# Optimization experiments

Hardware: AMD Instinct MI355X
Metric: run time of the kernel (lower is better)

The kernel has to match this reference:

```python
import jax, jax.numpy as jnp
import numpy as np

D_MODEL = 1024
NUM_HEADS = 16
HEAD_DIM = D_MODEL // NUM_HEADS
NEG_INF = -1e9


def setup_inputs() -> dict:
    key = jax.random.key(0)
    ks = jax.random.split(key, 9)
    B, S, SI = 4, 1024, 512
    scale = 1.0 / np.sqrt(D_MODEL)
    return {
        "hidden_states": jax.random.normal(ks[0], (B, S, D_MODEL), jnp.float32),
        "image_hidden_states": jax.random.normal(ks[1], (B, SI, D_MODEL), jnp.float32),
        "attention_mask": jax.random.randint(ks[2], (B, 1, S, S + SI), 0, 2, jnp.int32),
        "w_q": jax.random.normal(ks[3], (D_MODEL, D_MODEL), jnp.float32) * scale,
        "w_k": jax.random.normal(ks[4], (D_MODEL, D_MODEL), jnp.float32) * scale,
        "w_v": jax.random.normal(ks[5], (D_MODEL, D_MODEL), jnp.float32) * scale,
        "u_k": jax.random.normal(ks[6], (D_MODEL, D_MODEL), jnp.float32) * scale,
        "u_v": jax.random.normal(ks[7], (D_MODEL, D_MODEL), jnp.float32) * scale,
        "w_o": jax.random.normal(ks[8], (D_MODEL, D_MODEL), jnp.float32) * scale,
    }


def _split_heads(x):
    # [B, S, D] -> [B, H, S, Dh]
    B, S, _ = x.shape
    return x.reshape(B, S, NUM_HEADS, HEAD_DIM).transpose(0, 2, 1, 3)


def reference(hidden_states, image_hidden_states, attention_mask,
              w_q, w_k, w_v, u_k, u_v, w_o):
    # nn.Linear(bias=False): y = x @ W.T
    q = _split_heads(hidden_states @ w_q.T)          # [B,H,S,Dh]
    k = _split_heads(hidden_states @ w_k.T)          # [B,H,S,Dh]
    v = _split_heads(hidden_states @ w_v.T)
    k_img = _split_heads(image_hidden_states @ u_k.T)  # [B,H,SI,Dh]
    v_img = _split_heads(image_hidden_states @ u_v.T)
    k = jnp.concatenate([k, k_img], axis=2)          # [B,H,S+SI,Dh]
    v = jnp.concatenate([v, v_img], axis=2)

    scores = jnp.einsum('bhqd,bhkd->bhqk', q, k) / np.sqrt(HEAD_DIM)
    scores = jnp.where(attention_mask == 0, NEG_INF, scores)
    p_attn = jax.nn.softmax(scores, axis=-1)         # dropout p=0.0 (eval)
    x = jnp.einsum('bhqk,bhkd->bhqd', p_attn, v)     # [B,H,S,Dh]
    B, H, S, Dh = x.shape
    x = x.transpose(0, 2, 1, 3).reshape(B, S, D_MODEL)
    return x @ w_o.T
```

## Files before the change

### kernel.cpp

```cpp
#include <hip/hip_runtime.h>
#include <stdint.h>


typedef unsigned short u16;
typedef short bf16x8v __attribute__((ext_vector_type(8)));
typedef float f32x4 __attribute__((ext_vector_type(4)));

__device__ __forceinline__ u16 f2bf(float f) {
  union { float f; uint32_t u; } x; x.f = f;
  uint32_t r = x.u + 0x7FFFu + ((x.u >> 16) & 1u);
  return (u16)(r >> 16);
}

__device__ __forceinline__ uint32_t cvtpk(float a, float b) {
  uint32_t r;
  asm("v_cvt_pk_bf16_f32 %0, %1, %2" : "=v"(r) : "v"(a), "v"(b));
  return r;
}

__device__ __forceinline__ float maskand(float e, uint32_t msrc, int off) {
  uint32_t mm = (uint32_t)((int32_t)(msrc << (31 - off)) >> 31);
  union { float f; uint32_t u; } x; x.f = e; x.u &= mm; return x.f;
}

__device__ __forceinline__ void gl_lds16(const u16* g, u16* l) {
  __builtin_amdgcn_global_load_lds((const __attribute__((address_space(1))) unsigned int*)g,
                                   (__attribute__((address_space(3))) unsigned int*)l,
                                   16, 0, 0);
}

__global__ __launch_bounds__(512, 2) void gemm_qkv(
    const float* __restrict__ Hs, const float* __restrict__ Im,
    const float* __restrict__ Wq, const float* __restrict__ Wk, const float* __restrict__ Wv,
    const float* __restrict__ Uk, const float* __restrict__ Uv,
    const int* __restrict__ Mk,
    u16* __restrict__ Qd, u16* __restrict__ Kd, u16* __restrict__ Vd,
    uint32_t* __restrict__ Mw)
{
  __shared__ __align__(16) u16 As[2 * 16384];
  __shared__ __align__(16) u16 Bs[2 * 16384];
  const int hb = blockIdx.x;
  const int xcd = hb & 7, slot = hb >> 3;
  int bid = (slot < 24) ? xcd * 24 + slot : 192 + xcd * 8 + (slot - 24);
  const float *Ap, *Bp;
  int bm, bn, mode;
  if (bid < 192) { mode = 4; bm = (bid / 12) * 256; bn = (bid % 12) * 256;
                   Ap = Hs + (size_t)bm * 1024;
                   Bp = ((bn < 1024) ? Wq : (bn < 2048) ? Wk : Wv) + (size_t)(bn & 1023) * 1024; }
  else           { mode = 5; int r = bid - 192; bm = (r >> 3) * 256; bn = (r & 7) * 256;
                   Ap = Im + (size_t)bm * 1024;
                   Bp = ((bn < 1024) ? Uk : Uv) + (size_t)(bn & 1023) * 1024; }
  const int tid = threadIdx.x, lane = tid & 63, wave = tid >> 6;
  const int wr = wave >> 2, wc = wave & 3;
  const int g = lane >> 4, c = lane & 15, cs = c & 7;
  const int srow = tid >> 3;
  const int pch  = tid & 7;
  const int gsw  = (pch ^ (srow & 7)) * 8;

  f32x4 zf = {0.f, 0.f, 0.f, 0.f};
  f32x4 acc[8][4];
  #pragma unroll
  for (int f = 0; f < 8; ++f)
    #pragma unroll
    for (int nf = 0; nf < 4; ++nf) acc[f][nf] = zf;

  float4 sa[4][2], sb[4][2];

  #define LOAD_A(kt)                                                               \
    _Pragma("unroll")                                                              \
    for (int j_ = 0; j_ < 4; ++j_) {                                               \
      const float* p_ = Ap + (size_t)(j_ * 64 + srow) * 1024 + (kt) * 64 + gsw;    \
      sa[j_][0] = *(const float4*)p_;                                              \
      sa[j_][1] = *(const float4*)(p_ + 4);                                        \
    }
  #define LOAD_B(kt)                                                               \
    _Pragma("unroll")                                                              \
    for (int j_ = 0; j_ < 4; ++j_) {                                               \
      const float* p_ = Bp + (size_t)(j_ * 64 + srow) * 1024 + (kt) * 64 + gsw;    \
      sb[j_][0] = *(const float4*)p_;                                              \
      sb[j_][1] = *(const float4*)(p_ + 4);                                        \
    }
  #define CVT_A(buf)                                                               \
    _Pragma("unroll")                                                              \
    for (int j_ = 0; j_ < 4; ++j_) {                                               \
      uint4 w_;                                                                    \
      w_.x = cvtpk(sa[j_][0].x, sa[j_][0].y);                                      \
      w_.y = cvtpk(sa[j_][0].z, sa[j_][0].w);                                      \
      w_.z = cvtpk(sa[j_][1].x, sa[j_][1].y);                                      \
      w_.w = cvtpk(sa[j_][1].z, sa[j_][1].w);                                      \
      *(uint4*)&As[(buf) + (j_ * 64 + srow) * 64 + pch * 8] = w_;                  \
    }
  #define CVT_B(buf)                                                               \
    _Pragma("unroll")                                                              \
    for (int j_ = 0; j_ < 4; ++j_) {                                               \
      uint4 w_;                                                                    \
      w_.x = cvtpk(sb[j_][0].x, sb[j_][0].y);                                      \
      w_.y = cvtpk(sb[j_][0].z, sb[j_][0].w);                                      \
      w_.z = cvtpk(sb[j_][1].x, sb[j_][1].y);                                      \
      w_.w = cvtpk(sb[j_][1].z, sb[j_][1].w);                                      \
      *(uint4*)&Bs[(buf) + (j_ * 64 + srow) * 64 + pch * 8] = w_;                  \
    }

  LOAD_A(0); LOAD_B(0);
  {
    const int fid = hb * 512 + tid;
    #pragma unroll 1
    for (int w = fid; w < 196608; w += 131072) {
      const int4* p = (const int4*)(Mk + (size_t)w * 32);
      uint32_t bits = 0;
      #pragma unroll 1
      for (int h_ = 0; h_ < 2; ++h_) {
        int4 v0 = p[h_ * 4 + 0], v1 = p[h_ * 4 + 1];
        int4 v2 = p[h_ * 4 + 2], v3 = p[h_ * 4 + 3];
        int bo = h_ * 16;
        bits |= (uint32_t)(v0.x != 0) << (bo + 0);
        bits |= (uint32_t)(v0.y != 0) << (bo + 1);
        bits |= (uint32_t)(v0.z != 0) << (bo + 2);
        bits |= (uint32_t)(v0.w != 0) << (bo + 3);
        bits |= (uint32_t)(v1.x != 0) << (bo + 4);
        bits |= (uint32_t)(v1.y != 0) << (bo + 5);
        bits |= (uint32_t)(v1.z != 0) << (bo + 6);
        bits |= (uint32_t)(v1.w != 0) << (bo + 7);
        bits |= (uint32_t)(v2.x != 0) << (bo + 8);
        bits |= (uint32_t)(v2.y != 0) << (bo + 9);
        bits |= (uint32_t)(v2.z != 0) << (bo + 10);
        bits |= (uint32_t)(v2.w != 0) << (bo + 11);
        bits |= (uint32_t)(v3.x != 0) << (bo + 12);
        bits |= (uint32_t)(v3.y != 0) << (bo + 13);
        bits |= (uint32_t)(v3.z != 0) << (bo + 14);
        bits |= (uint32_t)(v3.w != 0) << (bo + 15);
      }
      Mw[w] = bits;
    }
  }
  CVT_A(0);  CVT_B(0);
  __syncthreads();

  for (int kt = 0; kt < 16; ++kt) {
    const int bc = (kt & 1) * 16384;
    const int bx = bc ^ 16384;
    if (kt < 15) LOAD_A(kt + 1);

    bf16x8v Bf[4][2];
    #pragma unroll
    for (int nf = 0; nf < 4; ++nf)
      #pragma unroll
      for (int ks = 0; ks < 2; ++ks)
        Bf[nf][ks] = *(const bf16x8v*)&Bs[bc + (wc * 64 + nf * 16 + c) * 64 + ((ks * 4 + g) ^ cs) * 8];

    #pragma unroll
    for (int p = 0; p < 4; ++p) {
      bf16x8v Af[2][2];
      #pragma unroll
      for (int i = 0; i < 2; ++i)
        #pragma unroll
        for (int ks = 0; ks < 2; ++ks)
          Af[i][ks] = *(const bf16x8v*)&As[bc + (wr * 128 + (p * 2 + i) * 16 + c) * 64 + ((ks * 4 + g) ^ cs) * 8];
      __builtin_amdgcn_s_setprio(1);
      #pragma unroll
      for (int i = 0; i < 2; ++i)
        #pragma unroll
        for (int nf = 0; nf < 4; ++nf)
          #pragma unroll
          for (int ks = 0; ks < 2; ++ks)
            acc[p * 2 + i][nf] =
              __builtin_amdgcn_mfma_f32_16x16x32_bf16(Af[i][ks], Bf[nf][ks], acc[p * 2 + i][nf], 0, 0, 0);
      __builtin_amdgcn_s_setprio(0);
      if (p == 1 && kt < 15) {
        __builtin_amdgcn_sched_barrier(0);
        CVT_A(bx);
        LOAD_B(kt + 1);
        __builtin_amdgcn_sched_barrier(0);
      }
    }
    if (kt < 15) {
      __builtin_amdgcn_sched_barrier(0);
      CVT_B(bx);
    }
    __syncthreads();
  }
  #undef LOAD_A
  #undef LOAD_B
  #undef CVT_A
  #undef CVT_B

  const int gn0 = bn + wc * 64;
  if (mode == 4) {
    if (bn < 1024) {
      #pragma unroll
      for (int f = 0; f < 8; ++f)
        #pragma unroll
        for (int nf = 0; nf < 4; ++nf) {
          int gm = bm + wr * 128 + f * 16 + 4 * g;
          int gn = gn0 + nf * 16 + c;
          #pragma unroll
          for (int j = 0; j < 4; ++j)
            Qd[(size_t)(gm + j) * 1024 + gn] = f2bf(acc[f][nf][j] * 0.18033688011112042f);
        }
    } else if (bn < 2048) {
      #pragma unroll
      for (int f = 0; f < 8; ++f)
        #pragma unroll
        for (int nf = 0; nf < 4; ++nf) {
          int gm = bm + wr * 128 + f * 16 + 4 * g;
          int b_ = gm >> 10, s_ = gm & 1023;
          int gn = gn0 - 1024 + nf * 16 + c;
          #pragma unroll
          for (int j = 0; j < 4; ++j)
            Kd[(size_t)(b_ * 1536 + s_ + j) * 1024 + gn] = f2bf(acc[f][nf][j]);
        }
    } else {
      #pragma unroll
      for (int f = 0; f < 8; ++f)
        #pragma unroll
        for (int nf = 0; nf < 4; ++nf) {
          int gm = bm + wr * 128 + f * 16 + 4 * g;
          int b_ = gm >> 10, s_ = gm & 1023;
          int d_ = gn0 - 2048 + nf * 16 + c;
          uint2 st;
          st.x = cvtpk(acc[f][nf][0], acc[f][nf][1]);
          st.y = cvtpk(acc[f][nf][2], acc[f][nf][3]);
          *(uint2*)&Vd[(size_t)(b_ * 1024 + d_) * 1536 + s_] = st;
        }
    }
  } else {
    if (bn < 1024) {
      #pragma unroll
      for (int f = 0; f < 8; ++f)
        #pragma unroll
        for (int nf = 0; nf < 4; ++nf) {
          int gm = bm + wr * 128 + f * 16 + 4 * g;
          int b_ = gm >> 9, s_ = gm & 511;
          int gn = gn0 + nf * 16 + c;
          #pragma unroll
          for (int j = 0; j < 4; ++j)
            Kd[(size_t)(b_ * 1536 + 1024 + s_ + j) * 1024 + gn] = f2bf(acc[f][nf][j]);
        }
    } else {
      #pragma unroll
      for (int f = 0; f < 8; ++f)
        #pragma unroll
        for (int nf = 0; nf < 4; ++nf) {
          int gm = bm + wr * 128 + f * 16 + 4 * g;
          int b_ = gm >> 9, s_ = gm & 511;
          int d_ = gn0 - 1024 + nf * 16 + c;
          uint2 st;
          st.x = cvtpk(acc[f][nf][0], acc[f][nf][1]);
          st.y = cvtpk(acc[f][nf][2], acc[f][nf][3]);
          *(uint2*)&Vd[(size_t)(b_ * 1024 + d_) * 1536 + 1024 + s_] = st;
        }
    }
  }
}

__global__ __launch_bounds__(256) void gemm_out(const u16* __restrict__ A, const float* __restrict__ Bw,
                                                float* __restrict__ Cout)
{
  __shared__ __align__(16) u16 As2[2 * 8192];
  __shared__ __align__(16) u16 Bs2[2 * 8192];
  const int hb = blockIdx.x;
  const int xcd = hb & 7, slot = hb >> 3;
  const int rg = xcd * 4 + (slot >> 3);
  const int cg = slot & 7;
  const int bm = rg * 128, bn = cg * 128;
  const int tid  = threadIdx.x;
  const int lane = tid & 63, wave = tid >> 6;
  const int wr = wave >> 1, wc = wave & 1;
  const int g = lane >> 4, c = lane & 15, cs = c & 7;
  const int sr  = tid >> 3;
  const int pch = tid & 7;
  const int gsw = (pch ^ (sr & 7)) * 8;

  f32x4 zf = {0.f, 0.f, 0.f, 0.f};
  f32x4 acc[4][4];
  #pragma unroll
  for (int mi = 0; mi < 4; ++mi)
    #pragma unroll
    for (int ni = 0; ni < 4; ++ni) acc[mi][ni] = zf;

  float4 sb[4][2];

  #define STG_A(buf, kt)                                                           \
    _Pragma("unroll")                                                              \
    for (int q_ = 0; q_ < 4; ++q_) {                                               \
      int row_ = q_ * 32 + sr;                                                     \
      gl_lds16(A + (size_t)(bm + row_) * 1024 + (kt) * 64 + gsw,                   \
               &As2[(buf) + row_ * 64 + pch * 8]);                                 \
    }
  #define LOAD_B(kt)                                                               \
    _Pragma("unroll")                                                              \
    for (int q_ = 0; q_ < 4; ++q_) {                                               \
      const float* p_ = Bw + (size_t)(bn + q_ * 32 + sr) * 1024 + (kt) * 64 + gsw; \
      sb[q_][0] = *(const float4*)p_;                                              \
      sb[q_][1] = *(const float4*)(p_ + 4);                                        \
    }
  #define CVT_B(buf)                                                               \
    _Pragma("unroll")                                                              \
    for (int q_ = 0; q_ < 4; ++q_) {                                               \
      uint4 w_;                                                                    \
      w_.x = cvtpk(sb[q_][0].x, sb[q_][0].y);                                      \
      w_.y = cvtpk(sb[q_][0].z, sb[q_][0].w);                                      \
      w_.z = cvtpk(sb[q_][1].x, sb[q_][1].y);                                      \
      w_.w = cvtpk(sb[q_][1].z, sb[q_][1].w);                                      \
      *(uint4*)&Bs2[(buf) + (q_ * 32 + sr) * 64 + pch * 8] = w_;                   \
    }

  STG_A(0, 0);
  LOAD_B(0);
  CVT_B(0);
  __syncthreads();

  for (int kt = 0; kt < 16; ++kt) {
    const int bc = (kt & 1) * 8192;
    const int bx = bc ^ 8192;
    if (kt < 15) { STG_A(bx, kt + 1); LOAD_B(kt + 1); }

    #pragma unroll
    for (int ks = 0; ks < 2; ++ks) {
      bf16x8v af[4], bfr[4];
      #pragma unroll
      for (int mi = 0; mi < 4; ++mi)
        af[mi] = *(const bf16x8v*)&As2[bc + (wr * 64 + mi * 16 + c) * 64 + ((ks * 4 + g) ^ cs) * 8];
      #pragma unroll
      for (int ni = 0; ni < 4; ++ni)
        bfr[ni] = *(const bf16x8v*)&Bs2[bc + (wc * 64 + ni * 16 + c) * 64 + ((ks * 4 + g) ^ cs) * 8];
      __builtin_amdgcn_s_setprio(1);
      #pragma unroll
      for (int mi = 0; mi < 4; ++mi)
        #pragma unroll
        for (int ni = 0; ni < 4; ++ni)
          acc[mi][ni] = __builtin_amdgcn_mfma_f32_16x16x32_bf16(af[mi], bfr[ni], acc[mi][ni], 0, 0, 0);
      __builtin_amdgcn_s_setprio(0);
    }
    if (kt < 15) {
      __builtin_amdgcn_sched_barrier(0);
      CVT_B(bx);
    }
    __syncthreads();
  }
  #undef STG_A
  #undef LOAD_B
  #undef CVT_B

  #pragma unroll
  for (int mi = 0; mi < 4; ++mi)
    #pragma unroll
    for (int ni = 0; ni < 4; ++ni)
      #pragma unroll
      for (int j = 0; j < 4; ++j) {
        int gm = bm + wr * 64 + mi * 16 + 4 * g + j;
        int gn = bn + wc * 64 + ni * 16 + c;
        Cout[(size_t)gm * 1024 + gn] = acc[mi][ni][j];
      }
}

__global__ __launch_bounds__(256) void attn_kernel(const u16* __restrict__ Q, const u16* __restrict__ Kc,
                                                   const u16* __restrict__ Vt,
                                                   const uint32_t* __restrict__ Mw,
                                                   u16* __restrict__ AO)
{
  const int bid = blockIdx.x;
  const int grp = bid & 63;
  const int qt  = bid >> 6;
  const int h = grp & 15, b = grp >> 4;
  const int q0 = qt * 64;
  const int tid = threadIdx.x, lane = tid & 63, wave = tid >> 6;
  const int g = lane >> 4, c = lane & 15;
  const int qw = q0 + wave * 16;

  __shared__ __align__(16) u16 Ks[64 * 64];
  __shared__ __align__(16) u16 Vs[64 * 64];
  __shared__ __align__(16) u16 Ps[4][16 * 72];

  bf16x8v qf0, qf1;
  {
    const u16* qp = Q + (size_t)(b * 1024 + qw + c) * 1024 + h * 64 + g * 8;
    qf0 = *(const bf16x8v*)qp;
    qf1 = *(const bf16x8v*)(qp + 32);
  }
  f32x4 zf = {0.f, 0.f, 0.f, 0.f};
  f32x4 O[4];
  float l = 0.f;
  #pragma unroll
  for (int dt = 0; dt < 4; ++dt) O[dt] = zf;

  const int sr  = tid >> 3;
  const int pch = tid & 7;
  const int swz = (pch ^ (sr & 7)) * 8;
  const int cs  = c & 7;
  const u16* Kbase = Kc + (size_t)(b * 1536) * 1024 + h * 64;
  const u16* Vbase = Vt + (size_t)(b * 1024 + h * 64) * 1536;
  const uint32_t* mrow = Mw + (size_t)(b * 1024 + qw + c) * 48;

  bf16x8v kr0, kr1, vr0, vr1;
  kr0 = *(const bf16x8v*)(Kbase + (size_t)sr * 1024 + pch * 8);
  kr1 = *(const bf16x8v*)(Kbase + (size_t)(32 + sr) * 1024 + pch * 8);
  vr0 = *(const bf16x8v*)(Vbase + (size_t)sr * 1536 + pch * 8);
  vr1 = *(const bf16x8v*)(Vbase + (size_t)(32 + sr) * 1536 + pch * 8);
  *(bf16x8v*)&Ks[sr * 64 + swz]        = kr0;
  *(bf16x8v*)&Ks[(32 + sr) * 64 + swz] = kr1;
  *(bf16x8v*)&Vs[sr * 64 + swz]        = vr0;
  *(bf16x8v*)&Vs[(32 + sr) * 64 + swz] = vr1;
  __syncthreads();

  for (int kt = 0; kt < 24; ++kt) {
    if (kt < 23) {
      const int ln = (kt + 1) * 64;
      kr0 = *(const bf16x8v*)(Kbase + (size_t)(ln + sr) * 1024 + pch * 8);
      kr1 = *(const bf16x8v*)(Kbase + (size_t)(ln + 32 + sr) * 1024 + pch * 8);
      vr0 = *(const bf16x8v*)(Vbase + (size_t)sr * 1536 + ln + pch * 8);
      vr1 = *(const bf16x8v*)(Vbase + (size_t)(32 + sr) * 1536 + ln + pch * 8);
    }
    uint2 mwv = *(const uint2*)(mrow + kt * 2);

    f32x4 s[4];
    __builtin_amdgcn_s_setprio(1);
    #pragma unroll
    for (int nt = 0; nt < 4; ++nt) {
      const u16* kr = &Ks[(nt * 16 + c) * 64];
      bf16x8v k0 = *(const bf16x8v*)&kr[(g ^ cs) * 8];
      bf16x8v k1 = *(const bf16x8v*)&kr[((4 + g) ^ cs) * 8];
      f32x4 z = zf;
      z = __builtin_amdgcn_mfma_f32_16x16x32_bf16(k0, qf0, z, 0, 0, 0);
      z = __builtin_amdgcn_mfma_f32_16x16x32_bf16(k1, qf1, z, 0, 0, 0);
      s[nt] = z;
    }
    __builtin_amdgcn_s_setprio(0);

    uint64_t mq = (((uint64_t)mwv.y << 32) | (uint64_t)mwv.x) >> (4 * g);
    uint32_t mlo = (uint32_t)mq, mhi = (uint32_t)(mq >> 32);
    #pragma unroll
    for (int nt = 0; nt < 4; ++nt) {
      uint32_t msrc = (nt < 2) ? mlo : mhi;
      #pragma unroll
      for (int j = 0; j < 4; ++j) {
        float e = exp2f(s[nt][j]);
        float p = maskand(e, msrc, 16 * (nt & 1) + j);
        s[nt][j] = p;
        l += p;
      }
    }

    u16* pw = &Ps[wave][0];
    #pragma unroll
    for (int nt = 0; nt < 4; ++nt) {
      uint2 pk2;
      pk2.x = cvtpk(s[nt][0], s[nt][1]);
      pk2.y = cvtpk(s[nt][2], s[nt][3]);
      *(uint2*)&pw[c * 72 + nt * 16 + g * 4] = pk2;
    }
    bf16x8v pb0 = *(const bf16x8v*)&pw[c * 72 + g * 8];
    bf16x8v pb1 = *(const bf16x8v*)&pw[c * 72 + 32 + g * 8];
    __builtin_amdgcn_s_setprio(1);
    #pragma unroll
    for (int dt = 0; dt < 4; ++dt) {
      const u16* vr = &Vs[(dt * 16 + c) * 64];
      bf16x8v v0 = *(const bf16x8v*)&vr[(g ^ cs) * 8];
      bf16x8v v1 = *(const bf16x8v*)&vr[((4 + g) ^ cs) * 8];
      O[dt] = __builtin_amdgcn_mfma_f32_16x16x32_bf16(v0, pb0, O[dt], 0, 0, 0);
      O[dt] = __builtin_amdgcn_mfma_f32_16x16x32_bf16(v1, pb1, O[dt], 0, 0, 0);
    }
    __builtin_amdgcn_s_setprio(0);

    __syncthreads();
    if (kt < 23) {
      *(bf16x8v*)&Ks[sr * 64 + swz]        = kr0;
      *(bf16x8v*)&Ks[(32 + sr) * 64 + swz] = kr1;
      *(bf16x8v*)&Vs[sr * 64 + swz]        = vr0;
      *(bf16x8v*)&Vs[(32 + sr) * 64 + swz] = vr1;
      __syncthreads();
    }
  }

  float r = l;
  r += __shfl_xor(r, 16);
  r += __shfl_xor(r, 32);
  float inv = 1.f / r;
  size_t ro = (size_t)(b * 1024 + qw + c) * 1024 + h * 64;
  #pragma unroll
  for (int dt = 0; dt < 4; ++dt) {
    uint2 st;
    st.x = cvtpk(O[dt][0] * inv, O[dt][1] * inv);
    st.y = cvtpk(O[dt][2] * inv, O[dt][3] * inv);
    *(uint2*)&AO[ro + dt * 16 + 4 * g] = st;
  }
}

extern "C" void kernel_launch(void* const* d_in, const int* in_sizes, int n_in,
                              void* d_out, int out_size, void* d_ws, size_t ws_size,
                              hipStream_t stream) {
  (void)in_sizes; (void)n_in; (void)out_size; (void)ws_size;
  const float* hs = (const float*)d_in[0];
  const float* im = (const float*)d_in[1];
  const int*   mk = (const int*)d_in[2];
  const float* wq = (const float*)d_in[3];
  const float* wk = (const float*)d_in[4];
  const float* wv = (const float*)d_in[5];
  const float* uk = (const float*)d_in[6];
  const float* uv = (const float*)d_in[7];
  const float* wo = (const float*)d_in[8];

  char* ws = (char*)d_ws;
  u16* Qb  = (u16*)(ws + 0);
  u16* Kb  = (u16*)(ws + 8388608);
  u16* Vtb = (u16*)(ws + 20971520);
  u16* AO  = (u16*)(ws + 33554432);
  uint32_t* Mw = (uint32_t*)(ws + 41943040);

  gemm_qkv<<<256, 512, 0, stream>>>(hs, im, wq, wk, wv, uk, uv, mk, Qb, Kb, Vtb, Mw);
  attn_kernel<<<1024, 256, 0, stream>>>(Qb, Kb, Vtb, Mw, AO);
  gemm_out<<<256, 256, 0, stream>>>(AO, wo, (float*)d_out);
}
```

Baseline: 133.7 us.

## Double-buffer attention K/V tiles via direct global-to-LDS loads; hoist GEMM B prefetch

The attention kernel now keeps two LDS buffers for K and V and fills the next tile with direct global-to-LDS loads (gl_lds16) while computing on the current one. This drops the register staging and one of the two barriers per iteration, and the swizzle moves from the LDS address to the global source address. The GEMM kernel also issues the B-tile prefetch at the top of the iteration next to the A prefetch, instead of midway through. The cost is twice the K/V LDS footprint, which may lower occupancy. The change also relies on a gl_lds16 helper that must already be defined in the hidden part of the file.

```diff
diff --git a/kernel.cpp b/kernel.cpp
--- a/kernel.cpp
+++ b/kernel.cpp
@@ -139,7 +139,7 @@
   for (int kt = 0; kt < 16; ++kt) {
     const int bc = (kt & 1) * 16384;
     const int bx = bc ^ 16384;
-    if (kt < 15) LOAD_A(kt + 1);
+    if (kt < 15) { LOAD_A(kt + 1); LOAD_B(kt + 1); }
 
     bf16x8v Bf[4][2];
     #pragma unroll
@@ -169,7 +169,6 @@
       if (p == 1 && kt < 15) {
         __builtin_amdgcn_sched_barrier(0);
         CVT_A(bx);
-        LOAD_B(kt + 1);
         __builtin_amdgcn_sched_barrier(0);
       }
     }
@@ -368,8 +367,8 @@
   const int g = lane >> 4, c = lane & 15;
   const int qw = q0 + wave * 16;
 
-  __shared__ __align__(16) u16 Ks[64 * 64];
-  __shared__ __align__(16) u16 Vs[64 * 64];
+  __shared__ __align__(16) u16 Ks[2][64 * 64];
+  __shared__ __align__(16) u16 Vs[2][64 * 64];
   __shared__ __align__(16) u16 Ps[4][16 * 72];
 
   bf16x8v qf0, qf1;
@@ -392,32 +391,27 @@
   const u16* Vbase = Vt + (size_t)(b * 1024 + h * 64) * 1536;
   const uint32_t* mrow = Mw + (size_t)(b * 1024 + qw + c) * 48;
 
-  bf16x8v kr0, kr1, vr0, vr1;
-  kr0 = *(const bf16x8v*)(Kbase + (size_t)sr * 1024 + pch * 8);
-  kr1 = *(const bf16x8v*)(Kbase + (size_t)(32 + sr) * 1024 + pch * 8);
-  vr0 = *(const bf16x8v*)(Vbase + (size_t)sr * 1536 + pch * 8);
-  vr1 = *(const bf16x8v*)(Vbase + (size_t)(32 + sr) * 1536 + pch * 8);
-  *(bf16x8v*)&Ks[sr * 64 + swz]        = kr0;
-  *(bf16x8v*)&Ks[(32 + sr) * 64 + swz] = kr1;
-  *(bf16x8v*)&Vs[sr * 64 + swz]        = vr0;
-  *(bf16x8v*)&Vs[(32 + sr) * 64 + swz] = vr1;
+  #define ATTN_STAGE(bf, l0)                                                      \
+    do {                                                                          \
+      gl_lds16(Kbase + (size_t)((l0) + sr) * 1024 + swz,      &Ks[bf][sr * 64 + pch * 8]);        \
+      gl_lds16(Kbase + (size_t)((l0) + 32 + sr) * 1024 + swz, &Ks[bf][(32 + sr) * 64 + pch * 8]); \
+      gl_lds16(Vbase + (size_t)sr * 1536 + (l0) + swz,        &Vs[bf][sr * 64 + pch * 8]);        \
+      gl_lds16(Vbase + (size_t)(32 + sr) * 1536 + (l0) + swz, &Vs[bf][(32 + sr) * 64 + pch * 8]); \
+    } while (0)
+
+  ATTN_STAGE(0, 0);
   __syncthreads();
 
   for (int kt = 0; kt < 24; ++kt) {
-    if (kt < 23) {
-      const int ln = (kt + 1) * 64;
-      kr0 = *(const bf16x8v*)(Kbase + (size_t)(ln + sr) * 1024 + pch * 8);
-      kr1 = *(const bf16x8v*)(Kbase + (size_t)(ln + 32 + sr) * 1024 + pch * 8);
-      vr0 = *(const bf16x8v*)(Vbase + (size_t)sr * 1536 + ln + pch * 8);
-      vr1 = *(const bf16x8v*)(Vbase + (size_t)(32 + sr) * 1536 + ln + pch * 8);
-    }
+    const int bc = kt & 1, bx = bc ^ 1;
+    if (kt < 23) ATTN_STAGE(bx, (kt + 1) * 64);
     uint2 mwv = *(const uint2*)(mrow + kt * 2);
 
     f32x4 s[4];
     __builtin_amdgcn_s_setprio(1);
     #pragma unroll
     for (int nt = 0; nt < 4; ++nt) {
-      const u16* kr = &Ks[(nt * 16 + c) * 64];
+      const u16* kr = &Ks[bc][(nt * 16 + c) * 64];
       bf16x8v k0 = *(const bf16x8v*)&kr[(g ^ cs) * 8];
       bf16x8v k1 = *(const bf16x8v*)&kr[((4 + g) ^ cs) * 8];
       f32x4 z = zf;
@@ -454,7 +448,7 @@
     __builtin_amdgcn_s_setprio(1);
     #pragma unroll
     for (int dt = 0; dt < 4; ++dt) {
-      const u16* vr = &Vs[(dt * 16 + c) * 64];
+      const u16* vr = &Vs[bc][(dt * 16 + c) * 64];
       bf16x8v v0 = *(const bf16x8v*)&vr[(g ^ cs) * 8];
       bf16x8v v1 = *(const bf16x8v*)&vr[((4 + g) ^ cs) * 8];
       O[dt] = __builtin_amdgcn_mfma_f32_16x16x32_bf16(v0, pb0, O[dt], 0, 0, 0);
@@ -462,15 +456,9 @@
     }
     __builtin_amdgcn_s_setprio(0);
 
-    __syncthreads();
-    if (kt < 23) {
-      *(bf16x8v*)&Ks[sr * 64 + swz]        = kr0;
-      *(bf16x8v*)&Ks[(32 + sr) * 64 + swz] = kr1;
-      *(bf16x8v*)&Vs[sr * 64 + swz]        = vr0;
-      *(bf16x8v*)&Vs[(32 + sr) * 64 + swz] = vr1;
-      __syncthreads();
-    }
-  }
+    if (kt < 23) __syncthreads();
+  }
+  #undef ATTN_STAGE
 
   float r = l;
   r += __shfl_xor(r, 16);
```

Result: slower. 151.4 us (+13.2%).

## Split attention over two key halves and merge the partial results

Applied to the files above, without the earlier changes.

The attention kernel now splits the 24 key tiles into two halves, launching twice as many blocks. Each block writes an unnormalized bf16 partial output and a per-row partial sum. A new merge kernel adds the two partials, divides by the combined sum, and writes the result into the reused Q buffer that the output GEMM then reads. The aim is more parallelism and shorter per-block serial loops, at the cost of an extra launch, roughly 16MB of extra partial traffic, and bf16 rounding of the unnormalized partials.

```diff
diff --git a/kernel.cpp b/kernel.cpp
--- a/kernel.cpp
+++ b/kernel.cpp
@@ -357,16 +357,21 @@
 __global__ __launch_bounds__(256) void attn_kernel(const u16* __restrict__ Q, const u16* __restrict__ Kc,
                                                    const u16* __restrict__ Vt,
                                                    const uint32_t* __restrict__ Mw,
-                                                   u16* __restrict__ AO)
+                                                   u16* __restrict__ Op0, u16* __restrict__ Op1,
+                                                   float* __restrict__ Lp0, float* __restrict__ Lp1)
 {
   const int bid = blockIdx.x;
   const int grp = bid & 63;
-  const int qt  = bid >> 6;
+  const int qt  = (bid >> 6) & 15;
+  const int half = bid >> 10;
   const int h = grp & 15, b = grp >> 4;
   const int q0 = qt * 64;
   const int tid = threadIdx.x, lane = tid & 63, wave = tid >> 6;
   const int g = lane >> 4, c = lane & 15;
   const int qw = q0 + wave * 16;
+  u16*  Op = half ? Op1 : Op0;
+  float* Lp = half ? Lp1 : Lp0;
+  const int kt0 = half * 12;
 
   __shared__ __align__(16) u16 Ks[64 * 64];
   __shared__ __align__(16) u16 Vs[64 * 64];
@@ -393,18 +398,21 @@
   const uint32_t* mrow = Mw + (size_t)(b * 1024 + qw + c) * 48;
 
   bf16x8v kr0, kr1, vr0, vr1;
-  kr0 = *(const bf16x8v*)(Kbase + (size_t)sr * 1024 + pch * 8);
-  kr1 = *(const bf16x8v*)(Kbase + (size_t)(32 + sr) * 1024 + pch * 8);
-  vr0 = *(const bf16x8v*)(Vbase + (size_t)sr * 1536 + pch * 8);
-  vr1 = *(const bf16x8v*)(Vbase + (size_t)(32 + sr) * 1536 + pch * 8);
+  {
+    const int l0 = kt0 * 64;
+    kr0 = *(const bf16x8v*)(Kbase + (size_t)(l0 + sr) * 1024 + pch * 8);
+    kr1 = *(const bf16x8v*)(Kbase + (size_t)(l0 + 32 + sr) * 1024 + pch * 8);
+    vr0 = *(const bf16x8v*)(Vbase + (size_t)sr * 1536 + l0 + pch * 8);
+    vr1 = *(const bf16x8v*)(Vbase + (size_t)(32 + sr) * 1536 + l0 + pch * 8);
+  }
   *(bf16x8v*)&Ks[sr * 64 + swz]        = kr0;
   *(bf16x8v*)&Ks[(32 + sr) * 64 + swz] = kr1;
   *(bf16x8v*)&Vs[sr * 64 + swz]        = vr0;
   *(bf16x8v*)&Vs[(32 + sr) * 64 + swz] = vr1;
   __syncthreads();
 
-  for (int kt = 0; kt < 24; ++kt) {
-    if (kt < 23) {
+  for (int kt = kt0; kt < kt0 + 12; ++kt) {
+    if (kt < kt0 + 11) {
       const int ln = (kt + 1) * 64;
       kr0 = *(const bf16x8v*)(Kbase + (size_t)(ln + sr) * 1024 + pch * 8);
       kr1 = *(const bf16x8v*)(Kbase + (size_t)(ln + 32 + sr) * 1024 + pch * 8);
@@ -463,7 +471,7 @@
     __builtin_amdgcn_s_setprio(0);
 
     __syncthreads();
-    if (kt < 23) {
+    if (kt < kt0 + 11) {
       *(bf16x8v*)&Ks[sr * 64 + swz]        = kr0;
       *(bf16x8v*)&Ks[(32 + sr) * 64 + swz] = kr1;
       *(bf16x8v*)&Vs[sr * 64 + swz]        = vr0;
@@ -475,15 +483,39 @@
   float r = l;
   r += __shfl_xor(r, 16);
   r += __shfl_xor(r, 32);
-  float inv = 1.f / r;
-  size_t ro = (size_t)(b * 1024 + qw + c) * 1024 + h * 64;
+  const int row = b * 1024 + qw + c;
+  if (lane < 16) Lp[(size_t)row * 16 + h] = r;
+  size_t ro = (size_t)row * 1024 + h * 64;
   #pragma unroll
   for (int dt = 0; dt < 4; ++dt) {
     uint2 st;
-    st.x = cvtpk(O[dt][0] * inv, O[dt][1] * inv);
-    st.y = cvtpk(O[dt][2] * inv, O[dt][3] * inv);
-    *(uint2*)&AO[ro + dt * 16 + 4 * g] = st;
-  }
+    st.x = cvtpk(O[dt][0], O[dt][1]);
+    st.y = cvtpk(O[dt][2], O[dt][3]);
+    *(uint2*)&Op[ro + dt * 16 + 4 * g] = st;
+  }
+}
+
+__global__ __launch_bounds__(256) void attn_merge(const u16* __restrict__ Op0, const u16* __restrict__ Op1,
+                                                  const float* __restrict__ Lp0, const float* __restrict__ Lp1,
+                                                  u16* __restrict__ AO)
+{
+  const int i = blockIdx.x * 256 + threadIdx.x;
+  const size_t flat = (size_t)i * 8;
+  const int row = i >> 7;
+  const int h = (i >> 3) & 15;
+  const float inv = 1.f / (Lp0[(size_t)row * 16 + h] + Lp1[(size_t)row * 16 + h]);
+  uint4 a = *(const uint4*)(Op0 + flat);
+  uint4 b = *(const uint4*)(Op1 + flat);
+  uint4 o;
+  #pragma unroll
+  for (int w = 0; w < 4; ++w) {
+    uint32_t au = (&a.x)[w], bu = (&b.x)[w];
+    union { uint32_t u; float f; } al, ah, bl, bh;
+    al.u = au << 16; ah.u = au & 0xFFFF0000u;
+    bl.u = bu << 16; bh.u = bu & 0xFFFF0000u;
+    (&o.x)[w] = cvtpk((al.f + bl.f) * inv, (ah.f + bh.f) * inv);
+  }
+  *(uint4*)(AO + flat) = o;
 }
 
 extern "C" void kernel_launch(void* const* d_in, const int* in_sizes, int n_in,
@@ -504,10 +536,14 @@
   u16* Qb  = (u16*)(ws + 0);
   u16* Kb  = (u16*)(ws + 8388608);
   u16* Vtb = (u16*)(ws + 20971520);
-  u16* AO  = (u16*)(ws + 33554432);
-  uint32_t* Mw = (uint32_t*)(ws + 41943040);
+  uint32_t* Mw = (uint32_t*)(ws + 33554432);
+  u16* Op0 = (u16*)(ws + 34340864);
+  u16* Op1 = (u16*)(ws + 42729472);
+  float* Lp0 = (float*)(ws + 51118080);
+  float* Lp1 = (float*)(ws + 51380224);
 
   gemm_qkv<<<256, 512, 0, stream>>>(hs, im, wq, wk, wv, uk, uv, mk, Qb, Kb, Vtb, Mw);
-  attn_kernel<<<1024, 256, 0, stream>>>(Qb, Kb, Vtb, Mw, AO);
-  gemm_out<<<256, 256, 0, stream>>>(AO, wo, (float*)d_out);
-}
+  attn_kernel<<<2048, 256, 0, stream>>>(Qb, Kb, Vtb, Mw, Op0, Op1, Lp0, Lp1);
+  attn_merge<<<4096, 256, 0, stream>>>(Op0, Op1, Lp0, Lp1, Qb);
+  gemm_out<<<256, 256, 0, stream>>>(Qb, wo, (float*)d_out);
+}
```

Result: slower. 140.9 us (+5.4%).
